# Optimization experiments

Measured on AMD Instinct MI355X. Metric: run time of the kernel, lower is better.

Reference implementation:

```python
import jax, jax.numpy as jnp
import numpy as np

B, N, K = 8, 2048, 20
CIN, COUT, DIM, PH, MULT, UP = 256, 128, 64, 64, 4, 2
EPS = 1e-5

def _lin(k, o, i):
    return jax.random.normal(k, (o, i), jnp.float32) * (1.0 / np.sqrt(i))

def setup_inputs() -> dict:
    key = jax.random.key(0)
    ks = jax.random.split(key, 32)
    H = DIM * MULT
    return {
        'pos': jax.random.normal(ks[0], (B, 3, N), jnp.float32),
        'key_feat': jax.random.normal(ks[1], (B, CIN, N), jnp.float32),
        'query_feat': jax.random.normal(ks[2], (B, CIN, N), jnp.float32),
        'upfeat': jax.random.normal(ks[3], (B, CIN, N), jnp.float32),
        'mv_w1': _lin(ks[4], CIN, 2 * CIN), 'mv_b1': jnp.zeros(CIN),
        'mv_w2': _lin(ks[5], CIN, CIN), 'mv_b2': jnp.zeros(CIN),
        'mv_ws': _lin(ks[6], CIN, 2 * CIN), 'mv_bs': jnp.zeros(CIN),
        'wk': _lin(ks[7], DIM, CIN), 'bk': jnp.zeros(DIM),
        'wq': _lin(ks[8], DIM, CIN), 'bq': jnp.zeros(DIM),
        'wv': _lin(ks[9], DIM, CIN), 'bv': jnp.zeros(DIM),
        'wu': _lin(ks[10], DIM, CIN), 'bu': jnp.zeros(DIM),
        'pm_w1': _lin(ks[11], PH, 3), 'pm_b1': jnp.zeros(PH),
        'pm_g': jnp.ones(PH) + 0.1 * jax.random.normal(ks[12], (PH,)),
        'pm_be': 0.1 * jax.random.normal(ks[13], (PH,)),
        'pm_m': 0.1 * jax.random.normal(ks[14], (PH,)),
        'pm_v': jax.random.uniform(ks[15], (PH,), minval=0.5, maxval=1.5),
        'pm_w2': _lin(ks[16], DIM, PH), 'pm_b2': jnp.zeros(DIM),
        'am_w1': _lin(ks[17], H, DIM), 'am_b1': jnp.zeros(H),
        'am_g': jnp.ones(H) + 0.1 * jax.random.normal(ks[18], (H,)),
        'am_be': 0.1 * jax.random.normal(ks[19], (H,)),
        'am_m': 0.1 * jax.random.normal(ks[20], (H,)),
        'am_v': jax.random.uniform(ks[21], (H,), minval=0.5, maxval=1.5),
        'am_wt': jax.random.normal(ks[22], (H, DIM, UP), jnp.float32) * (1.0 / np.sqrt(H)),
        'am_bt': jnp.zeros(DIM),
        'we': _lin(ks[23], COUT, DIM), 'be': jnp.zeros(COUT),
        'wr': _lin(ks[24], COUT, CIN), 'br': jnp.zeros(COUT),
    }

def _c1(x, w, b):  # 1x1 Conv1d: x (B,C,N)
    return jnp.einsum('oc,bcn->bon', w, x) + b[None, :, None]

def _c2(x, w, b):  # 1x1 Conv2d: x (B,C,N,K)
    return jnp.einsum('oc,bcnk->bonk', w, x) + b[None, :, None, None]

def _bn(x, g, be, m, v):  # eval-mode BatchNorm2d over channel dim
    sc = g / jnp.sqrt(v + EPS)
    return x * sc[None, :, None, None] + (be - m * sc)[None, :, None, None]

def _group(f, idx):  # f (B,C,N), idx (B,N,K) -> (B,C,N,K)
    return jax.vmap(lambda fb, ib: fb[:, ib])(f, idx)

def reference(pos, key_feat, query_feat, upfeat, mv_w1, mv_b1, mv_w2, mv_b2, mv_ws, mv_bs, wk, bk, wq, bq, wv, bv, wu, bu, pm_w1, pm_b1, pm_g, pm_be, pm_m, pm_v, pm_w2, pm_b2, am_w1, am_b1, am_g, am_be, am_m, am_v, am_wt, am_bt, we, be, wr, br):
    # mlp_v: MLP_Res(in=2*CIN, hidden=CIN, out=CIN)
    x = jnp.concatenate([key_feat, query_feat], axis=1)
    value = _c1(jax.nn.relu(_c1(x, mv_w1, mv_b1)), mv_w2, mv_b2) + _c1(x, mv_ws, mv_bs)
    identity = value
    k = _c1(key_feat, wk, bk)
    q = _c1(query_feat, wq, bq)
    v = _c1(value, wv, bv)
    # self-KNN on pos
    pt = jnp.swapaxes(pos, 1, 2)  # (B,N,3)
    sq = jnp.sum(pt * pt, -1)
    d2 = sq[:, :, None] + sq[:, None, :] - 2.0 * jnp.einsum('bnc,bmc->bnm', pt, pt)
    _, idx = jax.lax.top_k(-d2, K)  # (B,N,K)
    k_g = _group(k, idx)
    qk_rel = q[..., None] - k_g  # (B,DIM,N,K)
    pos_rel = pos[..., None] - _group(pos, idx)  # (B,3,N,K)
    pe = _c2(jax.nn.relu(_bn(_c2(pos_rel, pm_w1, pm_b1), pm_g, pm_be, pm_m, pm_v)), pm_w2, pm_b2)
    uf = _c1(upfeat, wu, bu)
    uf_rel = uf[..., None] - _group(uf, idx)
    # attn_mlp: conv2d -> BN -> ReLU -> ConvTranspose2d((UP,1),(UP,1))
    h = jax.nn.relu(_bn(_c2(qk_rel + pe + uf_rel, am_w1, am_b1), am_g, am_be, am_m, am_v))  # (B,H,N,K)
    attn = jnp.einsum('bcnk,cor->bonrk', h, am_wt)  # (B,DIM,N,UP,K)
    b_, o_, n_, r_, k_ = attn.shape
    attn = attn.reshape(b_, o_, n_ * r_, k_) + am_bt[None, :, None, None]  # (B,DIM,UP*N,K)
    attn = jax.nn.softmax(attn, axis=-1)  # scale_layer = Softmax(dim=-1)
    val = _group(v, idx) + pe + uf_rel  # (B,DIM,N,K)
    val = jnp.repeat(val, UP, axis=2)  # nearest Upsample (UP,1)
    agg = jnp.sum(attn * val, axis=-1)  # (B,DIM,UP*N)
    y = _c1(agg, we, be)
    iden = jnp.repeat(_c1(identity, wr, br), UP, axis=2)
    return y + iden
```

## Files before the change

### kernel.cpp

```cpp
#include <hip/hip_runtime.h>
#include <hip/hip_bf16.h>

constexpr int B_ = 8, N_ = 2048, K_ = 20;
constexpr float EPS_ = 1e-5f;

constexpr int OW1P = 0;
constexpr int OWSP = OW1P + 256 * 256;
constexpr int OW2P = OWSP + 256 * 256;
constexpr int OWVP = OW2P + 128 * 256;
constexpr int OWRP = OWVP + 128 * 64;
constexpr int OWQT = OWRP + 128 * 128;
constexpr int OWKT = OWQT + 256 * 64;
constexpr int OWUT = OWKT + 256 * 64;
constexpr int OWET = OWUT + 256 * 64;
constexpr int OWTF = OWET + 64 * 128;
constexpr int OAWF = OWTF + 16384;
constexpr int OPWF = OAWF + 8192;
constexpr int OPW1 = OPWF + 2048;
constexpr int OB1  = OPW1 + 192;
constexpr int OBS2 = OB1 + 256;
constexpr int OBQ  = OBS2 + 256;
constexpr int OBK  = OBQ + 64;
constexpr int OBV  = OBK + 64;
constexpr int OBU  = OBV + 64;
constexpr int OBR  = OBU + 64;
constexpr int OBE  = OBR + 128;
constexpr int OPB1 = OBE + 128;
constexpr int OPSC = OPB1 + 64;
constexpr int OPSH = OPSC + 64;
constexpr int OPB2 = OPSH + 64;
constexpr int OASC = OPB2 + 64;
constexpr int OASH = OASC + 256;
constexpr int OAB1 = OASH + 256;
constexpr int OABT = OAB1 + 256;

constexpr size_t OFFB_WF   = 0;
constexpr size_t OFFB_IDX  = (size_t)2 << 20;
constexpr size_t OFFB_Q    = (size_t)4 << 20;
constexpr size_t OFFB_K    = (size_t)8 << 20;
constexpr size_t OFFB_U    = (size_t)12 << 20;
constexpr size_t OFFB_V    = (size_t)16 << 20;
constexpr size_t OFFB_IDEN = (size_t)20 << 20;

struct InPtrs { const float* p[38]; };

typedef _Float16 half2_t __attribute__((ext_vector_type(2)));
typedef _Float16 f16x8_t __attribute__((ext_vector_type(8)));
typedef float    f32x4_t __attribute__((ext_vector_type(4)));

union U4H8 { uint4 u; f16x8_t h; };

__device__ __forceinline__ unsigned pkh2(float a, float b) {
  union { unsigned u; half2_t h; } x;
  x.h = half2_t{(_Float16)a, (_Float16)b};
  return x.u;
}
__device__ __forceinline__ f32x4_t mfma_16x16x32(f16x8_t a, f16x8_t b, f32x4_t c) {
  return __builtin_amdgcn_mfma_f32_16x16x32_f16(a, b, c, 0, 0, 0);
}

__global__ __launch_bounds__(256) void k_prep(InPtrs in, float* __restrict__ wf) {
  const int tid = blockIdx.x * 256 + threadIdx.x;
  const int nth = gridDim.x * 256;
  const float *mv_w1 = in.p[4], *mv_b1 = in.p[5], *mv_w2 = in.p[6], *mv_b2 = in.p[7],
              *mv_ws = in.p[8], *mv_bs = in.p[9], *wk = in.p[10], *bk = in.p[11],
              *wq = in.p[12], *bq = in.p[13], *wv = in.p[14], *bv = in.p[15],
              *wu = in.p[16], *bu = in.p[17], *pm_w1 = in.p[18], *pm_b1 = in.p[19],
              *pm_g = in.p[20], *pm_be = in.p[21], *pm_m = in.p[22], *pm_v = in.p[23],
              *pm_w2 = in.p[24], *pm_b2 = in.p[25], *am_w1 = in.p[26], *am_b1 = in.p[27],
              *am_g = in.p[28], *am_be = in.p[29], *am_m = in.p[30], *am_v = in.p[31],
              *am_wt = in.p[32], *am_bt = in.p[33], *we = in.p[34], *be = in.p[35],
              *wr = in.p[36], *br = in.p[37];

  {
    unsigned* w1f = (unsigned*)(wf + OW1P);
    for (int i = tid; i < 65536; i += nth) {
      int q = i & 3, l = (i >> 2) & 63, ks = (i >> 8) & 15, mt = i >> 12;
      int m = mt * 16 + (l & 15);
      int k = ks * 32 + ((l >> 4) << 3) + 2 * q;
      w1f[i] = pkh2(mv_w1[m * 512 + k], mv_w1[m * 512 + k + 1]);
    }
    unsigned* wsf = (unsigned*)(wf + OWSP);
    for (int i = tid; i < 65536; i += nth) {
      int q = i & 3, l = (i >> 2) & 63, ks = (i >> 8) & 15, mt = i >> 12;
      int m = mt * 16 + (l & 15);
      int k = ks * 32 + ((l >> 4) << 3) + 2 * q;
      wsf[i] = pkh2(mv_ws[m * 512 + k], mv_ws[m * 512 + k + 1]);
    }
    unsigned* w2f = (unsigned*)(wf + OW2P);
    for (int i = tid; i < 32768; i += nth) {
      int q = i & 3, l = (i >> 2) & 63, ks = (i >> 8) & 7, mt = i >> 11;
      int m = mt * 16 + (l & 15);
      int k = ks * 32 + ((l >> 4) << 3) + 2 * q;
      w2f[i] = pkh2(mv_w2[m * 256 + k], mv_w2[m * 256 + k + 1]);
    }
    unsigned* wvf = (unsigned*)(wf + OWVP);
    for (int i = tid; i < 8192; i += nth) {
      int q = i & 3, l = (i >> 2) & 63, ks = (i >> 8) & 7, mt = i >> 11;
      int m = mt * 16 + (l & 15);
      int k = ks * 32 + ((l >> 4) << 3) + 2 * q;
      wvf[i] = pkh2(wv[m * 256 + k], wv[m * 256 + k + 1]);
    }
    unsigned* wrf = (unsigned*)(wf + OWRP);
    for (int i = tid; i < 16384; i += nth) {
      int q = i & 3, l = (i >> 2) & 63, ks = (i >> 8) & 7, mt = i >> 11;
      int m = mt * 16 + (l & 15);
      int k = ks * 32 + ((l >> 4) << 3) + 2 * q;
      wrf[i] = pkh2(wr[m * 256 + k], wr[m * 256 + k + 1]);
    }
    unsigned* wqf = (unsigned*)(wf + OWQT);
    for (int i = tid; i < 8192; i += nth) {
      int q = i & 3, l = (i >> 2) & 63, ks = (i >> 8) & 7, mt = i >> 11;
      int m = mt * 16 + (l & 15);
      int k = ks * 32 + ((l >> 4) << 3) + 2 * q;
      wqf[i] = pkh2(wq[m * 256 + k], wq[m * 256 + k + 1]);
    }
    unsigned* wkf = (unsigned*)(wf + OWKT);
    for (int i = tid; i < 8192; i += nth) {
      int q = i & 3, l = (i >> 2) & 63, ks = (i >> 8) & 7, mt = i >> 11;
      int m = mt * 16 + (l & 15);
      int k = ks * 32 + ((l >> 4) << 3) + 2 * q;
      wkf[i] = pkh2(wk[m * 256 + k], wk[m * 256 + k + 1]);
    }
  }
  for (int i = tid; i < 256 * 64; i += nth) { int c = i >> 6, m = i & 63; wf[OWUT + i] = wu[m * 256 + c]; }
  for (int i = tid; i < 64 * 128; i += nth) wf[OWET + i] = we[i];

  {
    unsigned* wtf = (unsigned*)(wf + OWTF);
    for (int i = tid; i < 16384; i += nth) {
      int q = i & 3, l = (i >> 2) & 63, ks = (i >> 8) & 7, mt = i >> 11;
      int orr = mt * 16 + (l & 15);
      int c = ks * 32 + ((l >> 4) << 3) + 2 * q;
      wtf[i] = pkh2(am_wt[c * 128 + orr], am_wt[(c + 1) * 128 + orr]);
    }
  }
  {
    unsigned* awf = (unsigned*)(wf + OAWF);
    for (int i = tid; i < 8192; i += nth) {
      int q = i & 3, l = (i >> 2) & 63, ks = (i >> 8) & 1, mt = i >> 9;
      int c = mt * 16 + (l & 15);
      int o = ks * 32 + ((l >> 4) << 3) + 2 * q;
      awf[i] = pkh2(am_w1[c * 64 + o], am_w1[c * 64 + o + 1]);
    }
  }
  {
    unsigned* pwf = (unsigned*)(wf + OPWF);
    for (int i = tid; i < 2048; i += nth) {
      int q = i & 3, l = (i >> 2) & 63, ks = (i >> 8) & 1, mt = i >> 9;
      int o = mt * 16 + (l & 15);
      int ph = ks * 32 + ((l >> 4) << 3) + 2 * q;
      pwf[i] = pkh2(pm_w2[o * 64 + ph], pm_w2[o * 64 + ph + 1]);
    }
  }
  for (int i = tid; i < 192; i += nth) wf[OPW1 + i] = pm_w1[i];
  for (int i = tid; i < 256; i += nth) {
    wf[OB1 + i] = mv_b1[i];
    wf[OBS2 + i] = mv_bs[i] + mv_b2[i];
    float sc = am_g[i] / sqrtf(am_v[i] + EPS_);
    wf[OASC + i] = sc;
    wf[OASH + i] = am_be[i] - am_m[i] * sc;
    wf[OAB1 + i] = am_b1[i];
  }
  for (int i = tid; i < 64; i += nth) {
    wf[OBQ + i] = bq[i]; wf[OBK + i] = bk[i];
    wf[OBV + i] = bv[i]; wf[OBU + i] = bu[i];
    wf[OABT + i] = am_bt[i]; wf[OPB1 + i] = pm_b1[i]; wf[OPB2 + i] = pm_b2[i];
    float sc = pm_g[i] / sqrtf(pm_v[i] + EPS_);
    wf[OPSC + i] = sc;
    wf[OPSH + i] = pm_be[i] - pm_m[i] * sc;
  }
  for (int i = tid; i < 128; i += nth) { wf[OBR + i] = br[i]; wf[OBE + i] = be[i]; }
}

__global__ __launch_bounds__(256, 2) void k_mv(const float* __restrict__ wf,
                                               const float* __restrict__ keyf,
                                               const float* __restrict__ qryf,
                                               float* __restrict__ vout,
                                               float* __restrict__ idenout,
                                               float* __restrict__ qout,
                                               float* __restrict__ kout) {
  const int b = blockIdx.y;
  const int n0 = blockIdx.x * 32;
  const int tid = threadIdx.x, lane = tid & 63, wid = tid >> 6;
  __shared__ __align__(16) char smem[49152];
  char* xsb = smem;
  char* hbb = smem + 32768;
  char* vbb = smem;

  {
    const int col = tid & 31, kq = tid >> 5;
    const int swz = (col & 7) << 4;
#pragma unroll 4
    for (int it = 0; it < 32; ++it) {
      int k2 = it * 8 + kq;
      int c = 2 * k2;
      const float* s = (c < 256) ? keyf : qryf;
      size_t base = ((size_t)b * 256 + (c & 255)) * N_ + n0 + col;
      float x0 = s[base], x1 = s[base + N_];
      *(unsigned*)(xsb + ((col * 1024 + k2 * 4) ^ swz)) = pkh2(x0, x1);
    }
  }
  __syncthreads();

  f32x4_t acch[4][2], accs[4][2];
#pragma unroll
  for (int m = 0; m < 4; ++m)
#pragma unroll
    for (int nt = 0; nt < 2; ++nt) {
      acch[m][nt] = f32x4_t{0.f, 0.f, 0.f, 0.f};
      accs[m][nt] = f32x4_t{0.f, 0.f, 0.f, 0.f};
    }
  {
    const uint4* w1f = (const uint4*)((const unsigned*)(wf + OW1P));
    const uint4* wsf = (const uint4*)((const unsigned*)(wf + OWSP));
#pragma unroll 2
    for (int ks = 0; ks < 16; ++ks) {
      U4H8 bu[2];
#pragma unroll
      for (int nt = 0; nt < 2; ++nt) {
        int col = nt * 16 + (lane & 15);
        bu[nt].u = *(const uint4*)(xsb + ((col * 1024 + ks * 64 + ((lane >> 4) << 4)) ^ ((col & 7) << 4)));
      }
#pragma unroll
      for (int m = 0; m < 4; ++m) {
        U4H8 a1, as_;
        a1.u = w1f[((wid * 4 + m) * 16 + ks) * 64 + lane];
        as_.u = wsf[((wid * 4 + m) * 16 + ks) * 64 + lane];
#pragma unroll
        for (int nt = 0; nt < 2; ++nt) {
          acch[m][nt] = mfma_16x16x32(a1.h, bu[nt].h, acch[m][nt]);
          accs[m][nt] = mfma_16x16x32(as_.h, bu[nt].h, accs[m][nt]);
        }
      }
    }
  }
#pragma unroll
  for (int m = 0; m < 4; ++m) {
    int ch0 = (wid * 4 + m) * 16 + ((lane >> 4) << 2);
    float4 b1v = *(const float4*)(wf + OB1 + ch0);
#pragma unroll
    for (int nt = 0; nt < 2; ++nt) {
      int col = nt * 16 + (lane & 15);
      float h0 = fmaxf(acch[m][nt][0] + b1v.x, 0.f);
      float h1 = fmaxf(acch[m][nt][1] + b1v.y, 0.f);
      float h2 = fmaxf(acch[m][nt][2] + b1v.z, 0.f);
      float h3 = fmaxf(acch[m][nt][3] + b1v.w, 0.f);
      uint2 p;
      p.x = pkh2(h0, h1);
      p.y = pkh2(h2, h3);
      *(uint2*)(hbb + ((col * 512 + ch0 * 2) ^ ((col & 7) << 4))) = p;
    }
  }

  {
    f32x4_t accq[2], acck[2];
#pragma unroll
    for (int nt = 0; nt < 2; ++nt) {
      accq[nt] = f32x4_t{0.f, 0.f, 0.f, 0.f};
      acck[nt] = f32x4_t{0.f, 0.f, 0.f, 0.f};
    }
    const uint4* wqf = (const uint4*)((const unsigned*)(wf + OWQT));
    const uint4* wkf = (const uint4*)((const unsigned*)(wf + OWKT));
#pragma unroll 2
    for (int ks8 = 0; ks8 < 8; ++ks8) {
      U4H8 bk_[2], bq_[2];
#pragma unroll
      for (int nt = 0; nt < 2; ++nt) {
        int col = nt * 16 + (lane & 15);
        int swz = (col & 7) << 4;
        bk_[nt].u = *(const uint4*)(xsb + ((col * 1024 + ks8 * 64 + ((lane >> 4) << 4)) ^ swz));
        bq_[nt].u = *(const uint4*)(xsb + ((col * 1024 + (8 + ks8) * 64 + ((lane >> 4) << 4)) ^ swz));
      }
      U4H8 aq, ak;
      aq.u = wqf[(wid * 8 + ks8) * 64 + lane];
      ak.u = wkf[(wid * 8 + ks8) * 64 + lane];
#pragma unroll
      for (int nt = 0; nt < 2; ++nt) {
        acck[nt] = mfma_16x16x32(ak.h, bk_[nt].h, acck[nt]);
        accq[nt] = mfma_16x16x32(aq.h, bq_[nt].h, accq[nt]);
      }
    }
    int ch0 = wid * 16 + ((lane >> 4) << 2);
    float4 bqv = *(const float4*)(wf + OBQ + ch0);
    float4 bkv = *(const float4*)(wf + OBK + ch0);
#pragma unroll
    for (int nt = 0; nt < 2; ++nt) {
      int col = nt * 16 + (lane & 15);
      *(float4*)(qout + ((size_t)b * N_ + n0 + col) * 64 + ch0) =
          make_float4(accq[nt][0] + bqv.x, accq[nt][1] + bqv.y,
                      accq[nt][2] + bqv.z, accq[nt][3] + bqv.w);
      *(float4*)(kout + ((size_t)b * N_ + n0 + col) * 64 + ch0) =
          make_float4(acck[nt][0] + bkv.x, acck[nt][1] + bkv.y,
                      acck[nt][2] + bkv.z, acck[nt][3] + bkv.w);
    }
  }
  __syncthreads();

  {
    f32x4_t acc2[4][2];
#pragma unroll
    for (int m = 0; m < 4; ++m)
#pragma unroll
      for (int nt = 0; nt < 2; ++nt) acc2[m][nt] = f32x4_t{0.f, 0.f, 0.f, 0.f};
    const uint4* w2f = (const uint4*)((const unsigned*)(wf + OW2P));
#pragma unroll 2
    for (int ks = 0; ks < 8; ++ks) {
      U4H8 bu[2];
#pragma unroll
      for (int nt = 0; nt < 2; ++nt) {
        int col = nt * 16 + (lane & 15);
        bu[nt].u = *(const uint4*)(hbb + ((col * 512 + ks * 64 + ((lane >> 4) << 4)) ^ ((col & 7) << 4)));
      }
#pragma unroll
      for (int m = 0; m < 4; ++m) {
        U4H8 a2;
        a2.u = w2f[((wid * 4 + m) * 8 + ks) * 64 + lane];
#pragma unroll
        for (int nt = 0; nt < 2; ++nt)
          acc2[m][nt] = mfma_16x16x32(a2.h, bu[nt].h, acc2[m][nt]);
      }
    }
#pragma unroll
    for (int m = 0; m < 4; ++m) {
      int ch0 = (wid * 4 + m) * 16 + ((lane >> 4) << 2);
      float4 bsv = *(const float4*)(wf + OBS2 + ch0);
#pragma unroll
      for (int nt = 0; nt < 2; ++nt) {
        int col = nt * 16 + (lane & 15);
        float v0 = acc2[m][nt][0] + accs[m][nt][0] + bsv.x;
        float v1 = acc2[m][nt][1] + accs[m][nt][1] + bsv.y;
        float v2 = acc2[m][nt][2] + accs[m][nt][2] + bsv.z;
        float v3 = acc2[m][nt][3] + accs[m][nt][3] + bsv.w;
        uint2 p;
        p.x = pkh2(v0, v1);
        p.y = pkh2(v2, v3);
        *(uint2*)(vbb + ((col * 512 + ch0 * 2) ^ ((col & 7) << 4))) = p;
      }
    }
  }
  __syncthreads();

  {
    f32x4_t accv[2], accr[2][2];
#pragma unroll
    for (int nt = 0; nt < 2; ++nt) {
      accv[nt] = f32x4_t{0.f, 0.f, 0.f, 0.f};
      accr[0][nt] = f32x4_t{0.f, 0.f, 0.f, 0.f};
      accr[1][nt] = f32x4_t{0.f, 0.f, 0.f, 0.f};
    }
    const uint4* wvf = (const uint4*)((const unsigned*)(wf + OWVP));
    const uint4* wrf = (const uint4*)((const unsigned*)(wf + OWRP));
#pragma unroll 2
    for (int ks = 0; ks < 8; ++ks) {
      U4H8 bu[2];
#pragma unroll
      for (int nt = 0; nt < 2; ++nt) {
        int col = nt * 16 + (lane & 15);
        bu[nt].u = *(const uint4*)(vbb + ((col * 512 + ks * 64 + ((lane >> 4) << 4)) ^ ((col & 7) << 4)));
      }
      U4H8 av;
      av.u = wvf[(wid * 8 + ks) * 64 + lane];
#pragma unroll
      for (int nt = 0; nt < 2; ++nt)
        accv[nt] = mfma_16x16x32(av.h, bu[nt].h, accv[nt]);
#pragma unroll
      for (int m2 = 0; m2 < 2; ++m2) {
        U4H8 ar;
        ar.u = wrf[((wid * 2 + m2) * 8 + ks) * 64 + lane];
#pragma unroll
        for (int nt = 0; nt < 2; ++nt)
          accr[m2][nt] = mfma_16x16x32(ar.h, bu[nt].h, accr[m2][nt]);
      }
    }
    {
      int ch0 = wid * 16 + ((lane >> 4) << 2);
      float4 bvv = *(const float4*)(wf + OBV + ch0);
#pragma unroll
      for (int nt = 0; nt < 2; ++nt) {
        int col = nt * 16 + (lane & 15);
        *(float4*)(vout + ((size_t)b * N_ + n0 + col) * 64 + ch0) =
            make_float4(accv[nt][0] + bvv.x, accv[nt][1] + bvv.y,
                        accv[nt][2] + bvv.z, accv[nt][3] + bvv.w);
      }
    }
#pragma unroll
    for (int m2 = 0; m2 < 2; ++m2) {
      int ch0 = (wid * 2 + m2) * 16 + ((lane >> 4) << 2);
      float4 brv = *(const float4*)(wf + OBR + ch0);
#pragma unroll
      for (int nt = 0; nt < 2; ++nt) {
        int col = nt * 16 + (lane & 15);
        *(float4*)(idenout + ((size_t)b * N_ + n0 + col) * 128 + ch0) =
            make_float4(accr[m2][nt][0] + brv.x, accr[m2][nt][1] + brv.y,
                        accr[m2][nt][2] + brv.z, accr[m2][nt][3] + brv.w);
      }
    }
  }
}

__global__ __launch_bounds__(256) void k_gemm_u(const float* __restrict__ wf,
                                                const float* __restrict__ x,
                                                float* __restrict__ out) {
  const int b = blockIdx.y;
  const int n0 = blockIdx.x * 64;
  const float* Wt = wf + OWUT;
  const float* bias = wf + OBU;
  __shared__ float ws_[16][64];
  __shared__ float xs_[16][64];
  const int tid = threadIdx.x, tm = tid & 15, tn = tid >> 4;
  float acc[4][4] = {};
  for (int kt = 0; kt < 256; kt += 16) {
    for (int i = tid; i < 1024; i += 256) {
      int kk = i >> 6, col = i & 63;
      ws_[kk][col] = Wt[(size_t)(kt + kk) * 64 + col];
      xs_[kk][col] = x[((size_t)b * 256 + kt + kk) * N_ + n0 + col];
    }
    __syncthreads();
#pragma unroll
    for (int kk = 0; kk < 16; ++kk) {
      float4 x4 = *(const float4*)&xs_[kk][tn * 4];
      float4 w4 = *(const float4*)&ws_[kk][tm * 4];
      float wv[4] = {w4.x, w4.y, w4.z, w4.w};
      float xv[4] = {x4.x, x4.y, x4.z, x4.w};
#pragma unroll
      for (int i = 0; i < 4; ++i)
#pragma unroll
        for (int j = 0; j < 4; ++j) acc[i][j] += wv[i] * xv[j];
    }
    __syncthreads();
  }
#pragma unroll
  for (int j = 0; j < 4; ++j) {
    *(float4*)(out + ((size_t)b * N_ + n0 + tn * 4 + j) * 64 + tm * 4) =
        make_float4(acc[0][j] + bias[tm * 4], acc[1][j] + bias[tm * 4 + 1],
                    acc[2][j] + bias[tm * 4 + 2], acc[3][j] + bias[tm * 4 + 3]);
  }
}

__device__ __forceinline__ unsigned long long bitonic64_(unsigned long long v,
                                                         int lane) {
#pragma unroll
  for (int k = 2; k <= 64; k <<= 1) {
#pragma unroll
    for (int j = k >> 1; j > 0; j >>= 1) {
      unsigned long long o = (unsigned long long)__shfl_xor((long long)v, j);
      bool up = (lane & k) == 0;
      bool lower = (lane & j) == 0;
      bool keepmin = (lower == up);
      unsigned long long mn = o < v ? o : v;
      unsigned long long mx = o < v ? v : o;
      v = keepmin ? mn : mx;
    }
  }
  return v;
}

__global__ __launch_bounds__(256, 8) void k_knn(const float* __restrict__ pos,
                                                int* __restrict__ idxout) {
  const int b = blockIdx.x >> 11, n = blockIdx.x & 2047;
  __shared__ unsigned long long wkeys[4][20];
  __shared__ unsigned long long cand[4][64];
  const int tid = threadIdx.x;
  const int lane = tid & 63, wv = tid >> 6;
  const float* pb = pos + (size_t)b * 3 * N_;
  const double xq = pb[n], yq = pb[N_ + n], zq = pb[2 * N_ + n];
  const double sq = xq * xq + yq * yq + zq * zq;
  unsigned long long key[8];
#pragma unroll
  for (int s = 0; s < 8; ++s) {
    int i = tid + s * 256;
    double x = pb[i], y = pb[N_ + i], z = pb[2 * N_ + i];
    double psq = x * x + y * y + z * z;
    double dot = xq * x + yq * y + zq * z;
    double d2 = fmax((sq + psq) - 2.0 * dot, 0.0);
    key[s] = ((unsigned long long)__double_as_longlong(d2) & ~0x7FFull) |
             (unsigned long long)i;
  }
  unsigned long long m = key[0];
#pragma unroll
  for (int s = 1; s < 8; ++s) m = key[s] < m ? key[s] : m;

  unsigned long long v = bitonic64_(m, lane);
  unsigned long long T = (unsigned long long)__shfl((long long)v, 19);

  int c = 0;
#pragma unroll
  for (int s = 0; s < 8; ++s) c += (key[s] <= T) ? 1 : 0;
  int inc = c;
#pragma unroll
  for (int d = 1; d < 64; d <<= 1) {
    int t = __shfl_up(inc, d);
    if (lane >= d) inc += t;
  }
  const int C = __shfl(inc, 63);
  const int off = inc - c;

  if (C <= 64) {
    int o2 = off;
#pragma unroll
    for (int s = 0; s < 8; ++s) {
      if (key[s] <= T) { cand[wv][o2] = key[s]; ++o2; }
    }
    __builtin_amdgcn_wave_barrier();
    asm volatile("s_waitcnt lgkmcnt(0)" ::: "memory");
    unsigned long long cv = (lane < C) ? cand[wv][lane] : ~0ull;
    cv = bitonic64_(cv, lane);
    if (lane < K_) wkeys[wv][lane] = cv;
  } else {
    for (int r = 0; r < K_; ++r) {
      unsigned long long bk = key[0];
#pragma unroll
      for (int s = 1; s < 8; ++s) bk = key[s] < bk ? key[s] : bk;
      unsigned long long wk = bk;
#pragma unroll
      for (int mm = 32; mm; mm >>= 1) {
        unsigned long long ok = (unsigned long long)__shfl_xor((long long)wk, mm);
        if (ok < wk) wk = ok;
      }
      if (lane == 0) wkeys[wv][r] = wk;
      const int widx = (int)(wk & 0x7FF);
#pragma unroll
      for (int s = 0; s < 8; ++s)
        if (widx == tid + s * 256) key[s] = ~0ull;
    }
  }
  __syncthreads();

  if (tid < 128) {
    const int w = tid >> 5, p = tid & 31;
    if (p < 20) {
      const unsigned long long Kk = wkeys[w][p];
      int rank = p;
#pragma unroll
      for (int w2 = 0; w2 < 4; ++w2) {
        if (w2 == w) continue;
        int lo = 0, hi = 20;
        while (lo < hi) {
          int mid = (lo + hi) >> 1;
          if (wkeys[w2][mid] < Kk) lo = mid + 1; else hi = mid;
        }
        rank += lo;
      }
      if (rank < K_)
        idxout[((size_t)b * N_ + n) * K_ + rank] = (int)(Kk & 0x7FF);
    }
  }
}

__global__ __launch_bounds__(256, 6) void k_attn(
    const float* __restrict__ wf,
    const float* __restrict__ qb, const float* __restrict__ kb,
    const float* __restrict__ vb, const float* __restrict__ ub,
    const float* __restrict__ idenb, const int* __restrict__ idxb,
    const float* __restrict__ pos, float* __restrict__ out) {
  const int lb = ((int)blockIdx.x & 7) * 1024 + ((int)blockIdx.x >> 3);
  const int b = lb >> 10, n0 = (lb & 1023) * 2;
  const int tid = threadIdx.x;
  const int lane = tid & 63, wid = tid >> 6;

  __shared__ __align__(16) char smem[26784];
  char*  Sb   = smem;
  char*  t1b  = smem + 6144;
  char*  sb0  = smem + 12288;
  char*  hb   = smem + 6144;
  int*   idxs = (int*)(smem + 18432);
  float* prx  = (float*)(smem + 18592);
  float* pry  = (float*)(smem + 18752);
  float* prz  = (float*)(smem + 18912);
  float* lg   = (float*)smem;
  char*  svb  = smem + 20640;
  float* aggs = (float*)(smem + 25760);

  if (tid < 40) {
    int qi = tid >= 20;
    idxs[tid] = idxb[((size_t)b * N_ + n0 + qi) * K_ + (tid - qi * 20)] & 2047;
  }
  __syncthreads();

  {
    const int qi = wid >> 1;
    size_t rowq = ((size_t)b * N_ + n0 + qi) * 64;
    float qvo = qb[rowq + lane];
    float ufo = ub[rowq + lane];
#pragma unroll
    for (int t = 0; t < 10; ++t) {
      int col = wid * 10 + t;
      int j = idxs[col];
      size_t rowj = ((size_t)b * N_ + j) * 64;
      float kvv = kb[rowj + lane], vvv = vb[rowj + lane], uvv = ub[rowj + lane];
      float ur = ufo - uvv;
      int ro = (col * 128 + lane * 2) ^ ((col & 7) << 4);
      *(_Float16*)(sb0 + ro) = (_Float16)((qvo - kvv) + ur);
      *(_Float16*)(svb + ro) = (_Float16)(vvv + ur);
    }
    if (tid < 40) {
      int j = idxs[tid];
      int qn = n0 + (tid >= 20);
      const float* pp = pos + (size_t)b * 3 * N_;
      prx[tid] = pp[qn] - pp[j];
      pry[tid] = pp[N_ + qn] - pp[N_ + j];
      prz[tid] = pp[2 * N_ + qn] - pp[2 * N_ + j];
    }
  }
  __syncthreads();

  {
    int ph = lane;
    float w0 = wf[OPW1 + ph * 3], w1 = wf[OPW1 + ph * 3 + 1], w2 = wf[OPW1 + ph * 3 + 2];
    float pb1 = wf[OPB1 + ph], sc = wf[OPSC + ph], sh = wf[OPSH + ph];
#pragma unroll
    for (int t = 0; t < 10; ++t) {
      int col = wid * 10 + t;
      float u = pb1 + w0 * prx[col] + w1 * pry[col] + w2 * prz[col];
      float tv = fmaxf(u * sc + sh, 0.f);
      *(_Float16*)(t1b + ((col * 128 + ph * 2) ^ ((col & 7) << 4))) = (_Float16)tv;
    }
  }
  __syncthreads();

  {
    f32x4_t pacc[3];
#pragma unroll
    for (int nt = 0; nt < 3; ++nt) pacc[nt] = f32x4_t{0.f, 0.f, 0.f, 0.f};
    const int mt = wid;
#pragma unroll
    for (int ks = 0; ks < 2; ++ks) {
      U4H8 a;
      a.u = ((const uint4*)((const unsigned*)(wf + OPWF)))[(mt * 2 + ks) * 64 + lane];
#pragma unroll
      for (int nt = 0; nt < 3; ++nt) {
        int kc = nt * 16 + (lane & 15);
        U4H8 bu;
        bu.u = *(const uint4*)(t1b + ((kc * 128 + (ks * 32 + ((lane >> 4) << 3)) * 2) ^ ((kc & 7) << 4)));
        pacc[nt] = mfma_16x16x32(a.h, bu.h, pacc[nt]);
      }
    }
    const int o0 = mt * 16 + ((lane >> 4) << 2);
    float4 pb2v = *(const float4*)(wf + OPB2 + o0);
#pragma unroll
    for (int nt = 0; nt < 3; ++nt) {
      int kc = nt * 16 + (lane & 15);
      if (kc < 40) {
        int ro = (kc * 128 + o0 * 2) ^ ((kc & 7) << 4);
        float pe0 = pacc[nt][0] + pb2v.x, pe1 = pacc[nt][1] + pb2v.y;
        float pe2 = pacc[nt][2] + pb2v.z, pe3 = pacc[nt][3] + pb2v.w;
        const _Float16* sp = (const _Float16*)(sb0 + ro);
        _Float16* vp = (_Float16*)(svb + ro);
        uint2 ps, pv;
        ps.x = pkh2((float)sp[0] + pe0, (float)sp[1] + pe1);
        ps.y = pkh2((float)sp[2] + pe2, (float)sp[3] + pe3);
        pv.x = pkh2((float)vp[0] + pe0, (float)vp[1] + pe1);
        pv.y = pkh2((float)vp[2] + pe2, (float)vp[3] + pe3);
        *(uint2*)(Sb + ro) = ps;
        *(uint2*)vp = pv;
      }
    }
  }
  __syncthreads();

  f32x4_t acc5[2][3];
#pragma unroll
  for (int m = 0; m < 2; ++m)
#pragma unroll
    for (int nt = 0; nt < 3; ++nt) acc5[m][nt] = f32x4_t{0.f, 0.f, 0.f, 0.f};
#pragma unroll
  for (int c = 0; c < 2; ++c) {
    {
      f32x4_t acc[2][3];
#pragma unroll
      for (int m = 0; m < 2; ++m)
#pragma unroll
        for (int nt = 0; nt < 3; ++nt) acc[m][nt] = f32x4_t{0.f, 0.f, 0.f, 0.f};
#pragma unroll
      for (int ks = 0; ks < 2; ++ks) {
        U4H8 bfr[3];
#pragma unroll
        for (int nt = 0; nt < 3; ++nt) {
          int kc = nt * 16 + (lane & 15);
          bfr[nt].u = *(const uint4*)(Sb + ((kc * 128 + (ks * 32 + ((lane >> 4) << 3)) * 2) ^ ((kc & 7) << 4)));
        }
#pragma unroll
        for (int m = 0; m < 2; ++m) {
          U4H8 a;
          a.u = ((const uint4*)((const unsigned*)(wf + OAWF)))[((c * 8 + wid * 2 + m) * 2 + ks) * 64 + lane];
#pragma unroll
          for (int nt = 0; nt < 3; ++nt)
            acc[m][nt] = mfma_16x16x32(a.h, bfr[nt].h, acc[m][nt]);
        }
      }
#pragma unroll
      for (int m = 0; m < 2; ++m) {
        const int cg = (c * 8 + wid * 2 + m) * 16 + ((lane >> 4) << 2);
        const int cl = (wid * 2 + m) * 16 + ((lane >> 4) << 2);
        float4 ab1 = *(const float4*)(wf + OAB1 + cg);
        float4 asc = *(const float4*)(wf + OASC + cg);
        float4 ash = *(const float4*)(wf + OASH + cg);
#pragma unroll
        for (int nt = 0; nt < 3; ++nt) {
          int kc = nt * 16 + (lane & 15);
          float h0 = fmaxf((acc[m][nt][0] + ab1.x) * asc.x + ash.x, 0.f);
          float h1 = fmaxf((acc[m][nt][1] + ab1.y) * asc.y + ash.y, 0.f);
          float h2 = fmaxf((acc[m][nt][2] + ab1.z) * asc.z + ash.z, 0.f);
          float h3 = fmaxf((acc[m][nt][3] + ab1.w) * asc.w + ash.w, 0.f);
          uint2 p;
          p.x = pkh2(h0, h1);
          p.y = pkh2(h2, h3);
          *(uint2*)(hb + ((kc * 256 + cl * 2) ^ ((kc & 7) << 4))) = p;
        }
      }
    }
    __syncthreads();
    {
#pragma unroll
      for (int ksl = 0; ksl < 4; ++ksl) {
        U4H8 bfr[3];
#pragma unroll
        for (int nt = 0; nt < 3; ++nt) {
          int kc = nt * 16 + (lane & 15);
          bfr[nt].u = *(const uint4*)(hb + ((kc * 256 + (ksl * 32 + ((lane >> 4) << 3)) * 2) ^ ((kc & 7) << 4)));
        }
#pragma unroll
        for (int m = 0; m < 2; ++m) {
          U4H8 a;
          a.u = ((const uint4*)((const unsigned*)(wf + OWTF)))[((wid * 2 + m) * 8 + (c * 4 + ksl)) * 64 + lane];
#pragma unroll
          for (int nt = 0; nt < 3; ++nt)
            acc5[m][nt] = mfma_16x16x32(a.h, bfr[nt].h, acc5[m][nt]);
        }
      }
    }
    __syncthreads();
  }

#pragma unroll
  for (int m = 0; m < 2; ++m) {
    const int or0 = (wid * 2 + m) * 16 + ((lane >> 4) << 2);
#pragma unroll
    for (int nt = 0; nt < 3; ++nt) {
      int kc = nt * 16 + (lane & 15);
      if (kc < 40) {
#pragma unroll
        for (int r = 0; r < 4; ++r) lg[kc * 129 + or0 + r] = acc5[m][nt][r];
      }
    }
  }
  __syncthreads();

  {
    const int qsel = tid >> 7, orr = tid & 127, o = orr >> 1;
    float l[20];
#pragma unroll
    for (int kk = 0; kk < 20; ++kk) l[kk] = lg[(qsel * 20 + kk) * 129 + orr];
    float bt = wf[OABT + o];
    float m = -3.4e38f;
#pragma unroll
    for (int kk = 0; kk < 20; ++kk) { l[kk] += bt; m = fmaxf(m, l[kk]); }
    float s = 0.f;
#pragma unroll
    for (int kk = 0; kk < 20; ++kk) { l[kk] = expf(l[kk] - m); s += l[kk]; }
    float inv = 1.f / s;
    float a = 0.f;
#pragma unroll
    for (int kk = 0; kk < 20; ++kk) {
      int row = qsel * 20 + kk;
      a += l[kk] * (float)(*(const _Float16*)(svb + ((row * 128 + o * 2) ^ ((row & 7) << 4))));
    }
    aggs[qsel * 128 + orr] = a * inv;
  }
  __syncthreads();

  {
    const int co = tid & 127, r = tid >> 7;
    float y0 = wf[OBE + co], y1 = y0;
    const float* w = wf + OWET + co * 64;
#pragma unroll 4
    for (int o4 = 0; o4 < 16; ++o4) {
      float4 w4 = *(const float4*)(w + o4 * 4);
      const float wv[4] = {w4.x, w4.y, w4.z, w4.w};
#pragma unroll
      for (int j = 0; j < 4; ++j) {
        int oi = o4 * 4 + j;
        y0 += wv[j] * aggs[oi * 2 + r];
        y1 += wv[j] * aggs[128 + oi * 2 + r];
      }
    }
    float id0 = idenb[((size_t)b * N_ + n0) * 128 + co];
    float id1 = idenb[((size_t)b * N_ + n0 + 1) * 128 + co];
    size_t obase = ((size_t)b * 128 + co) * (size_t)(2 * N_);
    out[obase + 2 * n0 + r] = y0 + id0;
    out[obase + 2 * n0 + 2 + r] = y1 + id1;
  }
}

extern "C" void kernel_launch(void* const* d_in, const int* in_sizes, int n_in,
                              void* d_out, int out_size, void* d_ws, size_t ws_size,
                              hipStream_t stream) {
  (void)in_sizes; (void)n_in; (void)out_size; (void)ws_size;
  InPtrs ip;
  for (int i = 0; i < 38; ++i) ip.p[i] = (const float*)d_in[i];
  char* ws = (char*)d_ws;
  float* wf    = (float*)(ws + OFFB_WF);
  int*   idxb  = (int*)(ws + OFFB_IDX);
  float* qb    = (float*)(ws + OFFB_Q);
  float* kb    = (float*)(ws + OFFB_K);
  float* ubuf  = (float*)(ws + OFFB_U);
  float* vbuf  = (float*)(ws + OFFB_V);
  float* idenb = (float*)(ws + OFFB_IDEN);

  k_prep<<<dim3(256), dim3(256), 0, stream>>>(ip, wf);
  k_mv<<<dim3(64, 8), dim3(256), 0, stream>>>(wf, ip.p[1], ip.p[2], vbuf, idenb, qb, kb);
  k_gemm_u<<<dim3(32, 8), dim3(256), 0, stream>>>(wf, ip.p[3], ubuf);
  k_knn<<<dim3(B_ * N_), dim3(256), 0, stream>>>(ip.p[0], idxb);
  k_attn<<<dim3(B_ * N_ / 2), dim3(256), 0, stream>>>(wf, qb, kb, vbuf, ubuf, idenb, idxb,
                                                      ip.p[0], (float*)d_out);
}
```

Baseline: 490.7 us.

## Materialize full 256-channel hidden tile in LDS and drop chunked attn-MLP loop

Replaces the two-chunk attn_mlp loop (128 hidden channels per chunk, with two barriers each) with one pass that writes all 256 hidden channels to shared memory, then one 8-step transposed-conv MFMA loop. The LDS layout is reorganised so S is written in place instead of copied from a staging buffer. Padding rows (kc>=40) are clamped to row 0 so the smaller buffers are never read out of bounds. Shared memory grows to about 32KB and launch bounds drop from 6 to 5 blocks, trading occupancy for fewer barriers and less per-chunk overhead.

```diff
diff --git a/kernel.cpp b/kernel.cpp
--- a/kernel.cpp
+++ b/kernel.cpp
@@ -548,7 +548,7 @@
   }
 }
 
-__global__ __launch_bounds__(256, 6) void k_attn(
+__global__ __launch_bounds__(256, 5) void k_attn(
     const float* __restrict__ wf,
     const float* __restrict__ qb, const float* __restrict__ kb,
     const float* __restrict__ vb, const float* __restrict__ ub,
@@ -559,18 +559,17 @@
   const int tid = threadIdx.x;
   const int lane = tid & 63, wid = tid >> 6;
 
-  __shared__ __align__(16) char smem[26784];
+  __shared__ __align__(16) char smem[32384];
   char*  Sb   = smem;
-  char*  t1b  = smem + 6144;
-  char*  sb0  = smem + 12288;
-  char*  hb   = smem + 6144;
-  int*   idxs = (int*)(smem + 18432);
-  float* prx  = (float*)(smem + 18592);
-  float* pry  = (float*)(smem + 18752);
-  float* prz  = (float*)(smem + 18912);
+  char*  t1b  = smem + 5120;
+  char*  hb   = smem + 5120;
   float* lg   = (float*)smem;
-  char*  svb  = smem + 20640;
-  float* aggs = (float*)(smem + 25760);
+  char*  svb  = smem + 25600;
+  float* aggs = (float*)(smem + 30720);
+  int*   idxs = (int*)(smem + 31744);
+  float* prx  = (float*)(smem + 31904);
+  float* pry  = (float*)(smem + 32064);
+  float* prz  = (float*)(smem + 32224);
 
   if (tid < 40) {
     int qi = tid >= 20;
@@ -591,7 +590,7 @@
       float kvv = kb[rowj + lane], vvv = vb[rowj + lane], uvv = ub[rowj + lane];
       float ur = ufo - uvv;
       int ro = (col * 128 + lane * 2) ^ ((col & 7) << 4);
-      *(_Float16*)(sb0 + ro) = (_Float16)((qvo - kvv) + ur);
+      *(_Float16*)(Sb + ro) = (_Float16)((qvo - kvv) + ur);
       *(_Float16*)(svb + ro) = (_Float16)(vvv + ur);
     }
     if (tid < 40) {
@@ -631,8 +630,9 @@
 #pragma unroll
       for (int nt = 0; nt < 3; ++nt) {
         int kc = nt * 16 + (lane & 15);
+        int kr = kc < 40 ? kc : 0;
         U4H8 bu;
-        bu.u = *(const uint4*)(t1b + ((kc * 128 + (ks * 32 + ((lane >> 4) << 3)) * 2) ^ ((kc & 7) << 4)));
+        bu.u = *(const uint4*)(t1b + ((kr * 128 + (ks * 32 + ((lane >> 4) << 3)) * 2) ^ ((kr & 7) << 4)));
         pacc[nt] = mfma_16x16x32(a.h, bu.h, pacc[nt]);
       }
     }
@@ -645,60 +645,56 @@
         int ro = (kc * 128 + o0 * 2) ^ ((kc & 7) << 4);
         float pe0 = pacc[nt][0] + pb2v.x, pe1 = pacc[nt][1] + pb2v.y;
         float pe2 = pacc[nt][2] + pb2v.z, pe3 = pacc[nt][3] + pb2v.w;
-        const _Float16* sp = (const _Float16*)(sb0 + ro);
+        _Float16* sp = (_Float16*)(Sb + ro);
         _Float16* vp = (_Float16*)(svb + ro);
         uint2 ps, pv;
         ps.x = pkh2((float)sp[0] + pe0, (float)sp[1] + pe1);
         ps.y = pkh2((float)sp[2] + pe2, (float)sp[3] + pe3);
         pv.x = pkh2((float)vp[0] + pe0, (float)vp[1] + pe1);
         pv.y = pkh2((float)vp[2] + pe2, (float)vp[3] + pe3);
-        *(uint2*)(Sb + ro) = ps;
+        *(uint2*)sp = ps;
         *(uint2*)vp = pv;
       }
     }
   }
   __syncthreads();
 
-  f32x4_t acc5[2][3];
-#pragma unroll
-  for (int m = 0; m < 2; ++m)
-#pragma unroll
-    for (int nt = 0; nt < 3; ++nt) acc5[m][nt] = f32x4_t{0.f, 0.f, 0.f, 0.f};
-#pragma unroll
-  for (int c = 0; c < 2; ++c) {
-    {
-      f32x4_t acc[2][3];
-#pragma unroll
-      for (int m = 0; m < 2; ++m)
-#pragma unroll
-        for (int nt = 0; nt < 3; ++nt) acc[m][nt] = f32x4_t{0.f, 0.f, 0.f, 0.f};
-#pragma unroll
-      for (int ks = 0; ks < 2; ++ks) {
-        U4H8 bfr[3];
-#pragma unroll
-        for (int nt = 0; nt < 3; ++nt) {
-          int kc = nt * 16 + (lane & 15);
-          bfr[nt].u = *(const uint4*)(Sb + ((kc * 128 + (ks * 32 + ((lane >> 4) << 3)) * 2) ^ ((kc & 7) << 4)));
-        }
-#pragma unroll
-        for (int m = 0; m < 2; ++m) {
-          U4H8 a;
-          a.u = ((const uint4*)((const unsigned*)(wf + OAWF)))[((c * 8 + wid * 2 + m) * 2 + ks) * 64 + lane];
-#pragma unroll
-          for (int nt = 0; nt < 3; ++nt)
-            acc[m][nt] = mfma_16x16x32(a.h, bfr[nt].h, acc[m][nt]);
-        }
+#pragma unroll
+  for (int pass = 0; pass < 2; ++pass) {
+    const int mt0 = wid * 4 + pass * 2;
+    f32x4_t acc[2][3];
+#pragma unroll
+    for (int m = 0; m < 2; ++m)
+#pragma unroll
+      for (int nt = 0; nt < 3; ++nt) acc[m][nt] = f32x4_t{0.f, 0.f, 0.f, 0.f};
+#pragma unroll
+    for (int ks = 0; ks < 2; ++ks) {
+      U4H8 bfr[3];
+#pragma unroll
+      for (int nt = 0; nt < 3; ++nt) {
+        int kc = nt * 16 + (lane & 15);
+        int kr = kc < 40 ? kc : 0;
+        bfr[nt].u = *(const uint4*)(Sb + ((kr * 128 + (ks * 32 + ((lane >> 4) << 3)) * 2) ^ ((kr & 7) << 4)));
       }
 #pragma unroll
       for (int m = 0; m < 2; ++m) {
-        const int cg = (c * 8 + wid * 2 + m) * 16 + ((lane >> 4) << 2);
-        const int cl = (wid * 2 + m) * 16 + ((lane >> 4) << 2);
-        float4 ab1 = *(const float4*)(wf + OAB1 + cg);
-        float4 asc = *(const float4*)(wf + OASC + cg);
-        float4 ash = *(const float4*)(wf + OASH + cg);
-#pragma unroll
-        for (int nt = 0; nt < 3; ++nt) {
-          int kc = nt * 16 + (lane & 15);
+        U4H8 a;
+        a.u = ((const uint4*)((const unsigned*)(wf + OAWF)))[((mt0 + m) * 2 + ks) * 64 + lane];
+#pragma unroll
+        for (int nt = 0; nt < 3; ++nt)
+          acc[m][nt] = mfma_16x16x32(a.h, bfr[nt].h, acc[m][nt]);
+      }
+    }
+#pragma unroll
+    for (int m = 0; m < 2; ++m) {
+      const int c0 = (mt0 + m) * 16 + ((lane >> 4) << 2);
+      float4 ab1 = *(const float4*)(wf + OAB1 + c0);
+      float4 asc = *(const float4*)(wf + OASC + c0);
+      float4 ash = *(const float4*)(wf + OASH + c0);
+#pragma unroll
+      for (int nt = 0; nt < 3; ++nt) {
+        int kc = nt * 16 + (lane & 15);
+        if (kc < 40) {
           float h0 = fmaxf((acc[m][nt][0] + ab1.x) * asc.x + ash.x, 0.f);
           float h1 = fmaxf((acc[m][nt][1] + ab1.y) * asc.y + ash.y, 0.f);
           float h2 = fmaxf((acc[m][nt][2] + ab1.z) * asc.z + ash.z, 0.f);
@@ -706,42 +702,48 @@
           uint2 p;
           p.x = pkh2(h0, h1);
           p.y = pkh2(h2, h3);
-          *(uint2*)(hb + ((kc * 256 + cl * 2) ^ ((kc & 7) << 4))) = p;
+          *(uint2*)(hb + ((kc * 512 + c0 * 2) ^ ((kc & 7) << 4))) = p;
         }
       }
     }
+  }
+  __syncthreads();
+
+  {
+    f32x4_t acc5[2][3];
+#pragma unroll
+    for (int m = 0; m < 2; ++m)
+#pragma unroll
+      for (int nt = 0; nt < 3; ++nt) acc5[m][nt] = f32x4_t{0.f, 0.f, 0.f, 0.f};
+#pragma unroll
+    for (int ks = 0; ks < 8; ++ks) {
+      U4H8 bfr[3];
+#pragma unroll
+      for (int nt = 0; nt < 3; ++nt) {
+        int kc = nt * 16 + (lane & 15);
+        int kr = kc < 40 ? kc : 0;
+        bfr[nt].u = *(const uint4*)(hb + ((kr * 512 + (ks * 32 + ((lane >> 4) << 3)) * 2) ^ ((kr & 7) << 4)));
+      }
+#pragma unroll
+      for (int m = 0; m < 2; ++m) {
+        U4H8 a;
+        a.u = ((const uint4*)((const unsigned*)(wf + OWTF)))[((wid * 2 + m) * 8 + ks) * 64 + lane];
+#pragma unroll
+        for (int nt = 0; nt < 3; ++nt)
+          acc5[m][nt] = mfma_16x16x32(a.h, bfr[nt].h, acc5[m][nt]);
+      }
+    }
     __syncthreads();
-    {
-#pragma unroll
-      for (int ksl = 0; ksl < 4; ++ksl) {
-        U4H8 bfr[3];
-#pragma unroll
-        for (int nt = 0; nt < 3; ++nt) {
-          int kc = nt * 16 + (lane & 15);
-          bfr[nt].u = *(const uint4*)(hb + ((kc * 256 + (ksl * 32 + ((lane >> 4) << 3)) * 2) ^ ((kc & 7) << 4)));
+#pragma unroll
+    for (int m = 0; m < 2; ++m) {
+      const int or0 = (wid * 2 + m) * 16 + ((lane >> 4) << 2);
+#pragma unroll
+      for (int nt = 0; nt < 3; ++nt) {
+        int kc = nt * 16 + (lane & 15);
+        if (kc < 40) {
+#pragma unroll
+          for (int r = 0; r < 4; ++r) lg[kc * 129 + or0 + r] = acc5[m][nt][r];
         }
-#pragma unroll
-        for (int m = 0; m < 2; ++m) {
-          U4H8 a;
-          a.u = ((const uint4*)((const unsigned*)(wf + OWTF)))[((wid * 2 + m) * 8 + (c * 4 + ksl)) * 64 + lane];
-#pragma unroll
-          for (int nt = 0; nt < 3; ++nt)
-            acc5[m][nt] = mfma_16x16x32(a.h, bfr[nt].h, acc5[m][nt]);
-        }
-      }
-    }
-    __syncthreads();
-  }
-
-#pragma unroll
-  for (int m = 0; m < 2; ++m) {
-    const int or0 = (wid * 2 + m) * 16 + ((lane >> 4) << 2);
-#pragma unroll
-    for (int nt = 0; nt < 3; ++nt) {
-      int kc = nt * 16 + (lane & 15);
-      if (kc < 40) {
-#pragma unroll
-        for (int r = 0; r < 4; ++r) lg[kc * 129 + or0 + r] = acc5[m][nt][r];
       }
     }
   }
```

Result: faster. 451.1 us (-8.1%).
